# Optimization experiments

Measured on AMD Instinct MI355X. Metric: run time of the kernel, lower is better.

The kernel has to match this reference:

```python
import jax, jax.numpy as jnp
import numpy as np

N = 200000
H = 128        # n_heads == input feature dim
HID = 512      # hidden_features
D_H = 512      # scaling denominator
C = 10.0       # tanh clip scale


def setup_inputs() -> dict:
    key = jax.random.key(0)
    k0, k1, k2, k3, k4, k5 = jax.random.split(key, 6)
    output = jax.random.normal(k0, (N, H), dtype=jnp.float32)
    # adjacency row: binary mask (which nodes are reachable neighbors)
    adj_modified = (jax.random.uniform(k1, (N,)) < 0.5).astype(jnp.float32)
    W1 = jax.random.normal(k2, (HID, H), dtype=jnp.float32) * (1.0 / np.sqrt(H))
    b1 = jax.random.normal(k3, (HID,), dtype=jnp.float32) * 0.01
    W2 = jax.random.normal(k4, (HID, H), dtype=jnp.float32) * (1.0 / np.sqrt(H))
    b2 = jax.random.normal(k5, (HID,), dtype=jnp.float32) * 0.01
    return {"output": output, "adj_modified": adj_modified,
            "W1": W1, "b1": b1, "W2": W2, "b2": b2, "prev_node": 5}


def reference(output, adj_modified, W1, b1, W2, b2, prev_node):
    # v_i: [1, H] embedding of the previously selected node
    v_i = output[prev_node][None, :]
    # v_j: [N, H] neighbor embeddings gated by the adjacency row
    v_j = adj_modified[:, None] * output
    phi1_v_i = v_i @ W1.T + b1          # [1, HID]
    phi2_v_j = v_j @ W2.T + b2          # [N, HID]
    scores = (phi1_v_i @ phi2_v_j.T) / jnp.sqrt(jnp.asarray(D_H, jnp.float32))  # [1, N]
    attn = C * jnp.tanh(scores) * adj_modified  # clipped + masked, [1, N]
    attn = attn[0]                                # [N]
    w = jax.nn.softmax(attn, axis=0)
    w = w * (attn != 0).astype(w.dtype)
    p = w.max()
    selected_node = jnp.argmax(w)
    return selected_node, p
```

## Files before the change

### kernel.cpp

```cpp
#include <hip/hip_runtime.h>
#include <math.h>

#define NN 200000
#define H 128
#define HID 512

struct Ws {
    unsigned long long best;
    float Z;
    float s_b;
    float u[H];
};

__device__ __forceinline__ unsigned int fkey(float f) {
    unsigned int u = __float_as_uint(f);
    return (u & 0x80000000u) ? ~u : (u | 0x80000000u);
}
__device__ __forceinline__ float inv_fkey(unsigned int k) {
    return __uint_as_float((k & 0x80000000u) ? (k ^ 0x80000000u) : ~k);
}

__global__ __launch_bounds__(256)
void prep_kernel(const float* __restrict__ outp, const float* __restrict__ W1,
                 const float* __restrict__ b1, const float* __restrict__ W2,
                 const float* __restrict__ b2, const int* __restrict__ prev,
                 Ws* __restrict__ ws) {
    __shared__ float phi1_s[16];
    __shared__ float sb_s[16];
    __shared__ float u_s[256];
    int t = threadIdx.x;
    int lane = t & 63;
    int c = lane & 31;
    int hw = t >> 5;
    const float* vi = outp + (size_t)prev[0] * H;
    float4 v = ((const float4*)vi)[c];
#pragma unroll
    for (int r = 0; r < 2; ++r) {
        int kl = hw + r * 8;
        int k = blockIdx.x * 16 + kl;
        float4 w = ((const float4*)(W1 + (size_t)k * H))[c];
        float d = w.x * v.x + w.y * v.y + w.z * v.z + w.w * v.w;
        d += __shfl_xor(d, 16);
        d += __shfl_xor(d, 8);
        d += __shfl_xor(d, 4);
        d += __shfl_xor(d, 2);
        d += __shfl_xor(d, 1);
        if (c == 0) {
            float phi = d + b1[k];
            phi1_s[kl] = phi;
            sb_s[kl] = phi * b2[k];
        }
    }
    __syncthreads();
    if (t == 0) {
        float s = 0.f;
#pragma unroll
        for (int i = 0; i < 16; ++i) s += sb_s[i];
        atomicAdd(&ws->s_b, s);
    }
    int h = t & 127;
    int g = t >> 7;
    float up = 0.f;
#pragma unroll
    for (int kk = 0; kk < 8; ++kk) {
        int kl = g * 8 + kk;
        int k = blockIdx.x * 16 + kl;
        up += phi1_s[kl] * W2[(size_t)k * H + h];
    }
    u_s[t] = up;
    __syncthreads();
    if (t < 128) atomicAdd(&ws->u[h], u_s[t] + u_s[t + 128]);
}

__global__ __launch_bounds__(256)
void score_kernel(const float4* __restrict__ xv, const float* __restrict__ adj,
                  Ws* __restrict__ ws, int n) {
    __shared__ float zs[8];
    __shared__ unsigned long long bs[8];
    const float inv = 0.04419417382415922f;
    int t = threadIdx.x;
    int lane = t & 63;
    int c = lane & 31;
    int half = lane >> 5;
    int wib = t >> 6;
    int tlid = wib * 2 + half;
    float s_b = ws->s_b;
    float4 uv = ((const float4*)ws->u)[c];
    int gw = blockIdx.x * 4 + wib;
    int nw = gridDim.x * 4;
    int npairs = n >> 1;
    float zloc = 0.f;
    float bscore = -3.4e38f;
    int bidx = -1;
    for (int p = gw; p < npairs; p += nw) {
        int row = p * 2 + half;
        float4 x = xv[(size_t)row * 32 + c];
        float d = x.x * uv.x + x.y * uv.y + x.z * uv.z + x.w * uv.w;
        d += __shfl_xor(d, 16);
        d += __shfl_xor(d, 8);
        d += __shfl_xor(d, 4);
        d += __shfl_xor(d, 2);
        d += __shfl_xor(d, 1);
        if (c == 0) {
            float a = adj[row];
            float attn = 0.f;
            if (a != 0.f) {
                float score = (s_b + a * d) * inv;
                attn = 10.f * tanhf(score);
                if (score > bscore) { bscore = score; bidx = row; }
            }
            zloc += __expf(attn);
        }
    }
    if (c == 0) {
        zs[tlid] = zloc;
        unsigned long long pk = 0ull;
        if (bidx >= 0)
            pk = ((unsigned long long)fkey(bscore) << 32) |
                 (unsigned long long)(0xFFFFFFFFu - (unsigned int)bidx);
        bs[tlid] = pk;
    }
    __syncthreads();
    if (t == 0) {
        float z = 0.f;
        unsigned long long pk = 0ull;
#pragma unroll
        for (int i = 0; i < 8; ++i) { z += zs[i]; if (bs[i] > pk) pk = bs[i]; }
        atomicAdd(&ws->Z, z);
        atomicMax(&ws->best, pk);
    }
}

__global__ void final_kernel(const Ws* __restrict__ ws, float* __restrict__ outp) {
    unsigned long long b = ws->best;
    float Z = ws->Z;
    unsigned int idx = 0xFFFFFFFFu - (unsigned int)(b & 0xFFFFFFFFu);
    float score = inv_fkey((unsigned int)(b >> 32));
    float p = __expf(10.f * tanhf(score)) / Z;
    if (b == 0ull) { idx = 0; p = 0.f; }
    outp[0] = (float)idx;
    outp[1] = p;
}

extern "C" void kernel_launch(void* const* d_in, const int* in_sizes, int n_in,
                              void* d_out, int out_size, void* d_ws, size_t ws_size,
                              hipStream_t stream) {
    const float* outp = (const float*)d_in[0];
    const float* adj  = (const float*)d_in[1];
    const float* W1   = (const float*)d_in[2];
    const float* b1   = (const float*)d_in[3];
    const float* W2   = (const float*)d_in[4];
    const float* b2   = (const float*)d_in[5];
    const int*   prev = (const int*)d_in[6];
    int n = in_sizes[1];
    Ws* ws = (Ws*)d_ws;

    hipMemsetAsync(ws, 0, sizeof(Ws), stream);
    prep_kernel<<<32, 256, 0, stream>>>(outp, W1, b1, W2, b2, prev, ws);
    score_kernel<<<1024, 256, 0, stream>>>((const float4*)outp, adj, ws, n);
    final_kernel<<<1, 1, 0, stream>>>(ws, (float*)d_out);
}
```

Baseline: 192.1 us.

## Fold memset and final kernel into prep and last-block epilogue, batch row loads

The prep kernel now runs as a single 1024-thread block that writes u and s_b directly and zeroes the accumulators, which removes the memset launch and the atomics. The final kernel is folded into the score kernel through a last-block-done counter. Each warp now issues eight independent row loads before reducing them, to raise memory-level parallelism, and tanh is computed with an exp-based formula. A single-block prep kernel may take longer on its own than the previous 32-block version.

Measured after the change: 223.8 us. +16.5%, slower.

```diff
diff --git a/kernel.cpp b/kernel.cpp
--- a/kernel.cpp
+++ b/kernel.cpp
@@ -1,7 +1,6 @@
 #include <hip/hip_runtime.h>
 #include <math.h>
 
-#define NN 200000
 #define H 128
 #define HID 512
 
@@ -9,6 +8,7 @@
     unsigned long long best;
     float Z;
     float s_b;
+    unsigned int done;
     float u[H];
 };
 
@@ -20,24 +20,24 @@
     return __uint_as_float((k & 0x80000000u) ? (k ^ 0x80000000u) : ~k);
 }
 
-__global__ __launch_bounds__(256)
+__global__ __launch_bounds__(1024)
 void prep_kernel(const float* __restrict__ outp, const float* __restrict__ W1,
                  const float* __restrict__ b1, const float* __restrict__ W2,
                  const float* __restrict__ b2, const int* __restrict__ prev,
                  Ws* __restrict__ ws) {
-    __shared__ float phi1_s[16];
-    __shared__ float sb_s[16];
-    __shared__ float u_s[256];
+    __shared__ float phi1_s[HID];
+    __shared__ float sb_s[32];
+    __shared__ float u_part[8][H];
     int t = threadIdx.x;
     int lane = t & 63;
     int c = lane & 31;
-    int hw = t >> 5;
-    const float* vi = outp + (size_t)prev[0] * H;
-    float4 v = ((const float4*)vi)[c];
-#pragma unroll
-    for (int r = 0; r < 2; ++r) {
-        int kl = hw + r * 8;
-        int k = blockIdx.x * 16 + kl;
+    int g = t >> 5;
+    const float4* vi = (const float4*)(outp + (size_t)prev[0] * H);
+    float4 v = vi[c];
+    float sb = 0.f;
+#pragma unroll 4
+    for (int r = 0; r < 16; ++r) {
+        int k = g * 16 + r;
         float4 w = ((const float4*)(W1 + (size_t)k * H))[c];
         float d = w.x * v.x + w.y * v.y + w.z * v.z + w.w * v.w;
         d += __shfl_xor(d, 16);
@@ -47,99 +47,126 @@
         d += __shfl_xor(d, 1);
         if (c == 0) {
             float phi = d + b1[k];
-            phi1_s[kl] = phi;
-            sb_s[kl] = phi * b2[k];
+            phi1_s[k] = phi;
+            sb += phi * b2[k];
         }
     }
+    if (c == 0) sb_s[g] = sb;
     __syncthreads();
+    int h = t & 127;
+    int g2 = t >> 7;
+    float up = 0.f;
+#pragma unroll 8
+    for (int kk = 0; kk < 64; ++kk) {
+        int k = g2 * 64 + kk;
+        up += phi1_s[k] * W2[(size_t)k * H + h];
+    }
+    u_part[g2][h] = up;
+    __syncthreads();
+    if (t < H) {
+        float s = 0.f;
+#pragma unroll
+        for (int i = 0; i < 8; ++i) s += u_part[i][h];
+        ws->u[h] = s;
+    }
     if (t == 0) {
         float s = 0.f;
 #pragma unroll
-        for (int i = 0; i < 16; ++i) s += sb_s[i];
-        atomicAdd(&ws->s_b, s);
+        for (int i = 0; i < 32; ++i) s += sb_s[i];
+        ws->s_b = s;
+        ws->Z = 0.f;
+        ws->best = 0ull;
+        ws->done = 0u;
     }
-    int h = t & 127;
-    int g = t >> 7;
-    float up = 0.f;
-#pragma unroll
-    for (int kk = 0; kk < 8; ++kk) {
-        int kl = g * 8 + kk;
-        int k = blockIdx.x * 16 + kl;
-        up += phi1_s[kl] * W2[(size_t)k * H + h];
-    }
-    u_s[t] = up;
-    __syncthreads();
-    if (t < 128) atomicAdd(&ws->u[h], u_s[t] + u_s[t + 128]);
 }
 
 __global__ __launch_bounds__(256)
 void score_kernel(const float4* __restrict__ xv, const float* __restrict__ adj,
-                  Ws* __restrict__ ws, int n) {
-    __shared__ float zs[8];
-    __shared__ unsigned long long bs[8];
+                  Ws* __restrict__ ws, int n, int ntiles, int grid,
+                  float* __restrict__ outp) {
+    __shared__ float zs[4];
+    __shared__ unsigned long long bs[4];
     const float inv = 0.04419417382415922f;
     int t = threadIdx.x;
     int lane = t & 63;
     int c = lane & 31;
-    int half = lane >> 5;
-    int wib = t >> 6;
-    int tlid = wib * 2 + half;
+    int hv = lane >> 5;
+    int w = t >> 6;
     float s_b = ws->s_b;
     float4 uv = ((const float4*)ws->u)[c];
-    int gw = blockIdx.x * 4 + wib;
-    int nw = gridDim.x * 4;
-    int npairs = n >> 1;
     float zloc = 0.f;
     float bscore = -3.4e38f;
     int bidx = -1;
-    for (int p = gw; p < npairs; p += nw) {
-        int row = p * 2 + half;
-        float4 x = xv[(size_t)row * 32 + c];
-        float d = x.x * uv.x + x.y * uv.y + x.z * uv.z + x.w * uv.w;
-        d += __shfl_xor(d, 16);
-        d += __shfl_xor(d, 8);
-        d += __shfl_xor(d, 4);
-        d += __shfl_xor(d, 2);
-        d += __shfl_xor(d, 1);
-        if (c == 0) {
-            float a = adj[row];
-            float attn = 0.f;
-            if (a != 0.f) {
-                float score = (s_b + a * d) * inv;
-                attn = 10.f * tanhf(score);
-                if (score > bscore) { bscore = score; bidx = row; }
+    for (int tile = blockIdx.x; tile < ntiles; tile += grid) {
+        int base = tile * 64 + w * 16 + hv;
+        float4 x[8];
+#pragma unroll
+        for (int r = 0; r < 8; ++r) {
+            int row = base + 2 * r;
+            if (row >= n) row = n - 1;
+            x[r] = xv[(size_t)row * 32 + c];
+        }
+        float d[8];
+#pragma unroll
+        for (int r = 0; r < 8; ++r) {
+            float dd = x[r].x * uv.x + x[r].y * uv.y + x[r].z * uv.z + x[r].w * uv.w;
+            dd += __shfl_xor(dd, 16);
+            dd += __shfl_xor(dd, 8);
+            dd += __shfl_xor(dd, 4);
+            dd += __shfl_xor(dd, 2);
+            dd += __shfl_xor(dd, 1);
+            d[r] = dd;
+        }
+        if (c < 8) {
+            int row = base + 2 * c;
+            if (row < n) {
+                float dm = d[0];
+#pragma unroll
+                for (int r = 1; r < 8; ++r) dm = (c == r) ? d[r] : dm;
+                float a = adj[row];
+                float attn = 0.f;
+                if (a != 0.f) {
+                    float score = (s_b + a * dm) * inv;
+                    float e = __expf(2.f * score);
+                    attn = 10.f * ((e - 1.f) / (e + 1.f));
+                    if (score > bscore) { bscore = score; bidx = row; }
+                }
+                zloc += __expf(attn);
             }
-            zloc += __expf(attn);
         }
     }
-    if (c == 0) {
-        zs[tlid] = zloc;
-        unsigned long long pk = 0ull;
-        if (bidx >= 0)
-            pk = ((unsigned long long)fkey(bscore) << 32) |
-                 (unsigned long long)(0xFFFFFFFFu - (unsigned int)bidx);
-        bs[tlid] = pk;
+#pragma unroll
+    for (int m = 32; m >= 1; m >>= 1) zloc += __shfl_xor(zloc, m);
+    unsigned long long pk = 0ull;
+    if (bidx >= 0)
+        pk = ((unsigned long long)fkey(bscore) << 32) |
+             (unsigned long long)(0xFFFFFFFFu - (unsigned int)bidx);
+#pragma unroll
+    for (int m = 32; m >= 1; m >>= 1) {
+        unsigned long long o = __shfl_xor(pk, m);
+        if (o > pk) pk = o;
     }
+    if (lane == 0) { zs[w] = zloc; bs[w] = pk; }
     __syncthreads();
     if (t == 0) {
-        float z = 0.f;
-        unsigned long long pk = 0ull;
+        float z = zs[0] + zs[1] + zs[2] + zs[3];
+        unsigned long long p2 = bs[0];
 #pragma unroll
-        for (int i = 0; i < 8; ++i) { z += zs[i]; if (bs[i] > pk) pk = bs[i]; }
+        for (int i = 1; i < 4; ++i) if (bs[i] > p2) p2 = bs[i];
         atomicAdd(&ws->Z, z);
-        atomicMax(&ws->best, pk);
+        atomicMax(&ws->best, p2);
+        __threadfence();
+        if (atomicAdd(&ws->done, 1u) == (unsigned)(grid - 1)) {
+            unsigned long long b = atomicMax(&ws->best, 0ull);
+            float Z = atomicAdd(&ws->Z, 0.f);
+            unsigned int idx = 0xFFFFFFFFu - (unsigned int)(b & 0xFFFFFFFFu);
+            float score = inv_fkey((unsigned int)(b >> 32));
+            float p = __expf(10.f * tanhf(score)) / Z;
+            if (b == 0ull) { idx = 0; p = 0.f; }
+            outp[0] = (float)idx;
+            outp[1] = p;
+        }
     }
-}
-
-__global__ void final_kernel(const Ws* __restrict__ ws, float* __restrict__ outp) {
-    unsigned long long b = ws->best;
-    float Z = ws->Z;
-    unsigned int idx = 0xFFFFFFFFu - (unsigned int)(b & 0xFFFFFFFFu);
-    float score = inv_fkey((unsigned int)(b >> 32));
-    float p = __expf(10.f * tanhf(score)) / Z;
-    if (b == 0ull) { idx = 0; p = 0.f; }
-    outp[0] = (float)idx;
-    outp[1] = p;
 }
 
 extern "C" void kernel_launch(void* const* d_in, const int* in_sizes, int n_in,
@@ -155,8 +182,10 @@
     int n = in_sizes[1];
     Ws* ws = (Ws*)d_ws;
 
-    hipMemsetAsync(ws, 0, sizeof(Ws), stream);
-    prep_kernel<<<32, 256, 0, stream>>>(outp, W1, b1, W2, b2, prev, ws);
-    score_kernel<<<1024, 256, 0, stream>>>((const float4*)outp, adj, ws, n);
-    final_kernel<<<1, 1, 0, stream>>>(ws, (float*)d_out);
+    int ntiles = (n + 63) / 64;
+    int grid = 1042;
+
+    prep_kernel<<<1, 1024, 0, stream>>>(outp, W1, b1, W2, b2, prev, ws);
+    score_kernel<<<grid, 256, 0, stream>>>((const float4*)outp, adj, ws, n,
+                                           ntiles, grid, (float*)d_out);
 }
```
